# Kernel tuning notes

Measured on AMD Instinct MI355X. Metric: run time of the kernel, lower is better.

Reference implementation:

```python
import jax, jax.numpy as jnp
import numpy as np

N = 32768
E = 524288
B = 128
D = 256


def setup_inputs() -> dict:
    key = jax.random.key(0)
    ks = jax.random.split(key, 8)
    b_z = jax.random.normal(ks[0], (N, D), dtype=jnp.float32)
    src = jax.random.randint(ks[1], (E,), 0, N, dtype=jnp.int32)
    dst = jax.random.randint(ks[2], (E,), 0, N, dtype=jnp.int32)
    b_edge_weight = jax.random.uniform(ks[3], (E,), dtype=jnp.float32)
    # Glorot-ish init for layer weights (256->128->64->1)
    W1 = jax.random.normal(ks[4], (256, 128), dtype=jnp.float32) / np.sqrt(256)
    W2 = jax.random.normal(ks[5], (128, 64), dtype=jnp.float32) / np.sqrt(128)
    W3 = jax.random.normal(ks[6], (64, 1), dtype=jnp.float32) / np.sqrt(64)
    b1 = jnp.zeros((128,), jnp.float32)
    b2 = jnp.zeros((64,), jnp.float32)
    b3 = jnp.zeros((1,), jnp.float32)
    return {"b_z": b_z, "src": src, "dst": dst, "b_edge_weight": b_edge_weight,
            "W1": W1, "b1": b1, "W2": W2, "b2": b2, "W3": W3, "b3": b3,
            "b_size": B}


def _degree_norms(src, dst, n):
    ones = jnp.ones(src.shape[0], jnp.float32)
    out_deg = jax.ops.segment_sum(ones, src, num_segments=n)
    in_deg = jax.ops.segment_sum(ones, dst, num_segments=n)
    # DGL GraphConv norm='both': unweighted degrees, clamped to 1
    return jnp.clip(out_deg, 1.0) ** -0.5, jnp.clip(in_deg, 1.0) ** -0.5


def _gcn_layer(x, src, dst, ew, norm_src, norm_dst, W, b, use_tanh):
    # norm='both': scale source features, transform first (in_feats > out_feats),
    # weighted neighbor sum, then scale by in-degree norm, add bias, activate.
    h = (x * norm_src[:, None]) @ W            # [N, out]
    m = h[src] * ew[:, None]                   # [E, out] gathered messages
    agg = jax.ops.segment_sum(m, dst, num_segments=x.shape[0])  # [N, out]
    out = agg * norm_dst[:, None] + b
    return jnp.tanh(out) if use_tanh else out


def reference(b_z, src, dst, b_edge_weight, W1, b1, W2, b2, W3, b3, b_size):
    norm_src, norm_dst = _degree_norms(src, dst, b_z.shape[0])
    h = _gcn_layer(b_z, src, dst, b_edge_weight, norm_src, norm_dst, W1, b1, True)
    h = _gcn_layer(h, src, dst, b_edge_weight, norm_src, norm_dst, W2, b2, True)
    h = _gcn_layer(h, src, dst, b_edge_weight, norm_src, norm_dst, W3, b3, False)
    return h.reshape(b_size, -1)
```

## Files before the change

kernel.cpp:

```cpp
#include <hip/hip_runtime.h>


#define NB 128
#define NW4 8192

typedef unsigned int uint32;
typedef unsigned short ushort_t;
typedef __attribute__((ext_vector_type(8))) short bf16x8;
typedef __attribute__((ext_vector_type(4))) float f32x4;

__device__ inline ushort_t f2bf(float f) {
  uint32 u = __float_as_uint(f);
  u += 0x7fffu + ((u >> 16) & 1u);
  return (ushort_t)(u >> 16);
}
__device__ inline float bf2f(ushort_t h) { return __uint_as_float(((uint32)h) << 16); }


__global__ __launch_bounds__(1024) void lds_hist_kernel(const int* __restrict__ src,
                                                        const int* __restrict__ dst,
                                                        uint32* __restrict__ part_src,
                                                        uint32* __restrict__ part_dst,
                                                        int e, int epb) {
  __shared__ uint32 hs[NW4];
  __shared__ uint32 hd[NW4];
  const int t = threadIdx.x;
  for (int w = t; w < NW4; w += 1024) {
    hs[w] = 0;
    hd[w] = 0;
  }
  __syncthreads();
  const int base = blockIdx.x * epb;
  for (int k = t; k < epb; k += 1024) {
    int i = base + k;
    if (i < e) {
      int s = src[i], d = dst[i];
      atomicAdd(&hs[s >> 2], 1u << ((s & 3) * 8));
      atomicAdd(&hd[d >> 2], 1u << ((d & 3) * 8));
    }
  }
  __syncthreads();
  uint32* ps = part_src + (size_t)blockIdx.x * NW4;
  uint32* pd = part_dst + (size_t)blockIdx.x * NW4;
  for (int w = t; w < NW4; w += 1024) {
    ps[w] = hs[w];
    pd[w] = hd[w];
  }
}

__global__ void reduce_norm_kernel(const uint32* __restrict__ part_src,
                                   const uint32* __restrict__ part_dst,
                                   float* __restrict__ norm_src, float* __restrict__ norm_dst,
                                   int* __restrict__ in_deg, int n4) {
  int w = blockIdx.x * blockDim.x + threadIdx.x;
  if (w >= n4) return;
  uint32 ss = 0, sd = 0;
  for (int r = 0; r < NB; ++r) {
    ss += part_src[(size_t)r * n4 + w];
    sd += part_dst[(size_t)r * n4 + w];
  }
#pragma unroll
  for (int j = 0; j < 4; ++j) {
    int v = w * 4 + j;
    int od = (ss >> (j * 8)) & 0xff;
    int id = (sd >> (j * 8)) & 0xff;
    norm_src[v] = 1.0f / sqrtf((float)max(od, 1));
    norm_dst[v] = 1.0f / sqrtf((float)max(id, 1));
    in_deg[v] = id;
  }
}

__global__ __launch_bounds__(256) void scan_partials_a(const int* __restrict__ deg,
                                                       int* __restrict__ block_sums, int n) {
  const int t = threadIdx.x;
  const int gid = blockIdx.x * 256 + t;
  int d = (gid < n) ? deg[gid] : 0;
#pragma unroll
  for (int off = 32; off > 0; off >>= 1) d += __shfl_down(d, off, 64);
  __shared__ int wsum[4];
  if ((t & 63) == 0) wsum[t >> 6] = d;
  __syncthreads();
  if (t == 0) block_sums[blockIdx.x] = wsum[0] + wsum[1] + wsum[2] + wsum[3];
}

__global__ __launch_bounds__(256) void scan_partials_b(int* __restrict__ block_sums,
                                                       int* __restrict__ block_offs, int nb) {
  __shared__ int sh[256];
  const int t = threadIdx.x;
  sh[t] = (t < nb) ? block_sums[t] : 0;
  __syncthreads();
  for (int off = 1; off < 256; off <<= 1) {
    int v = sh[t];
    int add = (t >= off) ? sh[t - off] : 0;
    __syncthreads();
    sh[t] = v + add;
    __syncthreads();
  }
  if (t < nb) block_offs[t] = (t > 0) ? sh[t - 1] : 0;
}

__global__ __launch_bounds__(256) void scan_write(const int* __restrict__ deg,
                                                  const int* __restrict__ block_offs,
                                                  int* __restrict__ row_ptr, int n) {
  __shared__ int sh[256];
  const int t = threadIdx.x;
  const int gid = blockIdx.x * 256 + t;
  int d = (gid < n) ? deg[gid] : 0;
  sh[t] = d;
  __syncthreads();
  for (int off = 1; off < 256; off <<= 1) {
    int v = sh[t];
    int add = (t >= off) ? sh[t - off] : 0;
    __syncthreads();
    sh[t] = v + add;
    __syncthreads();
  }
  if (gid < n) {
    int excl = block_offs[blockIdx.x] + sh[t] - d;
    row_ptr[gid] = excl;
    if (gid == n - 1) row_ptr[n] = excl + d;
  }
}

__global__ void group_offs_kernel(const uint32* __restrict__ part_dst,
                                  const int* __restrict__ row_ptr,
                                  int* __restrict__ goff, int n) {
  int v = blockIdx.x * blockDim.x + threadIdx.x;
  if (v >= n) return;
  int base = row_ptr[v];
  const int w = v >> 2;
  const int sh = (v & 3) * 8;
  const int n4 = n >> 2;
  for (int r = 0; r < NB; ++r) {
    goff[(size_t)r * n + v] = base;
    base += (part_dst[(size_t)r * n4 + w] >> sh) & 0xff;
  }
}

__global__ __launch_bounds__(1024) void scatter_kernel(const int* __restrict__ src,
                                                       const int* __restrict__ dst,
                                                       const float* __restrict__ ew,
                                                       const int* __restrict__ goff,
                                                       int2* __restrict__ csr,
                                                       int n, int e, int epb) {
  __shared__ uint32 rk[NW4];
  const int t = threadIdx.x;
  for (int w = t; w < NW4; w += 1024) rk[w] = 0;
  __syncthreads();
  const int base = blockIdx.x * epb;
  const int* gof = goff + (size_t)blockIdx.x * n;
  for (int k = t; k < epb; k += 1024) {
    int i = base + k;
    if (i < e) {
      int d = dst[i];
      uint32 sh = (d & 3) * 8;
      uint32 old = atomicAdd(&rk[d >> 2], 1u << sh);
      int rank = (old >> sh) & 0xff;
      csr[gof[d] + rank] = make_int2(src[i], __float_as_int(ew[i]));
    }
  }
}

__global__ void wsplit_kernel(const float* __restrict__ W, ushort_t* __restrict__ WhT,
                              ushort_t* __restrict__ WlT, int K, int OUT) {
  int i = blockIdx.x * blockDim.x + threadIdx.x;
  if (i >= K * OUT) return;
  int k = i / OUT, c = i % OUT;
  float f = W[i];
  ushort_t h = f2bf(f);
  ushort_t l = f2bf(f - bf2f(h));
  WhT[(size_t)c * K + k] = h;
  WlT[(size_t)c * K + k] = l;
}

template <int K, int OUT>
__global__ __launch_bounds__(256) void gemm_mfma(const float* __restrict__ x,
                                                 const ushort_t* __restrict__ WhT,
                                                 const ushort_t* __restrict__ WlT,
                                                 const float* __restrict__ norm_src,
                                                 ushort_t* __restrict__ ht, int n) {
  constexpr int BK = 64, KP = BK + 8;
  constexpr int NCT = OUT / 32;
  __shared__ ushort_t Xh[64][KP], Xl[64][KP];
  __shared__ ushort_t Wh[OUT][KP], Wl[OUT][KP];

  const int tid = threadIdx.x;
  const int wv = tid >> 6;
  const int lane = tid & 63;
  const int wr = wv >> 1;
  const int wc = wv & 1;
  const int row0 = blockIdx.x * 64;
  const int fr = lane & 15;
  const int fg = lane >> 4;

  f32x4 acc[2][NCT];
#pragma unroll
  for (int i = 0; i < 2; ++i)
#pragma unroll
    for (int j = 0; j < NCT; ++j) acc[i][j] = (f32x4){0.f, 0.f, 0.f, 0.f};

#pragma unroll 1
  for (int k0 = 0; k0 < K; k0 += BK) {
    __syncthreads();
#pragma unroll
    for (int p = 0; p < 4; ++p) {
      int idx = p * 256 + tid;
      int r = idx >> 4, c4 = idx & 15;
      float4 v = *reinterpret_cast<const float4*>(x + (size_t)(row0 + r) * K + k0 + c4 * 4);
      ushort4 h, l;
      h.x = f2bf(v.x); l.x = f2bf(v.x - bf2f(h.x));
      h.y = f2bf(v.y); l.y = f2bf(v.y - bf2f(h.y));
      h.z = f2bf(v.z); l.z = f2bf(v.z - bf2f(h.z));
      h.w = f2bf(v.w); l.w = f2bf(v.w - bf2f(h.w));
      *reinterpret_cast<ushort4*>(&Xh[r][c4 * 4]) = h;
      *reinterpret_cast<ushort4*>(&Xl[r][c4 * 4]) = l;
    }
#pragma unroll
    for (int p = 0; p < OUT * 16 / 256; ++p) {
      int idx = p * 256 + tid;
      int c = idx >> 4, k4 = idx & 15;
      *reinterpret_cast<ushort4*>(&Wh[c][k4 * 4]) =
          *reinterpret_cast<const ushort4*>(WhT + (size_t)c * K + k0 + k4 * 4);
      *reinterpret_cast<ushort4*>(&Wl[c][k4 * 4]) =
          *reinterpret_cast<const ushort4*>(WlT + (size_t)c * K + k0 + k4 * 4);
    }
    __syncthreads();

#pragma unroll
    for (int s = 0; s < 2; ++s) {
      const int kk = s * 32 + fg * 8;
      bf16x8 ah[2], al[2];
#pragma unroll
      for (int i = 0; i < 2; ++i) {
        int r = wr * 32 + i * 16 + fr;
        ah[i] = *reinterpret_cast<const bf16x8*>(&Xh[r][kk]);
        al[i] = *reinterpret_cast<const bf16x8*>(&Xl[r][kk]);
      }
#pragma unroll
      for (int j = 0; j < NCT; ++j) {
        int c = wc * (OUT / 2) + j * 16 + fr;
        bf16x8 bh = *reinterpret_cast<const bf16x8*>(&Wh[c][kk]);
        bf16x8 bl = *reinterpret_cast<const bf16x8*>(&Wl[c][kk]);
#pragma unroll
        for (int i = 0; i < 2; ++i) {
          acc[i][j] = __builtin_amdgcn_mfma_f32_16x16x32_bf16(ah[i], bh, acc[i][j], 0, 0, 0);
          acc[i][j] = __builtin_amdgcn_mfma_f32_16x16x32_bf16(ah[i], bl, acc[i][j], 0, 0, 0);
          acc[i][j] = __builtin_amdgcn_mfma_f32_16x16x32_bf16(al[i], bh, acc[i][j], 0, 0, 0);
        }
      }
    }
  }

#pragma unroll
  for (int i = 0; i < 2; ++i) {
#pragma unroll
    for (int q = 0; q < 4; ++q) {
      int row = row0 + wr * 32 + i * 16 + fg * 4 + q;
      float ns = norm_src[row];
#pragma unroll
      for (int j = 0; j < NCT; ++j) {
        int col = wc * (OUT / 2) + j * 16 + fr;
        ht[(size_t)row * OUT + col] = f2bf(acc[i][j][q] * ns);
      }
    }
  }
}

#define GATHB(e, acc)                                                               \
  {                                                                                 \
    float w_ = __int_as_float(e.y);                                                 \
    ushort4 h_ = *reinterpret_cast<const ushort4*>(ht + (size_t)e.x * OUT + cg * 4);\
    acc.x += w_ * bf2f(h_.x);                                                       \
    acc.y += w_ * bf2f(h_.y);                                                       \
    acc.z += w_ * bf2f(h_.z);                                                       \
    acc.w += w_ * bf2f(h_.w);                                                       \
  }

template <int OUT>
__global__ void aggregate_kernel(const ushort_t* __restrict__ ht, const int* __restrict__ row_ptr,
                                 const int2* __restrict__ csr, const float* __restrict__ norm_dst,
                                 const float* __restrict__ bias, float* __restrict__ out, int n) {
  constexpr int LPN = OUT / 4;
  constexpr int NPB = 256 / LPN;
  const int tid = threadIdx.x;
  const int cg = tid % LPN;
  const int v = blockIdx.x * NPB + tid / LPN;
  if (v >= n) return;

  const int s0 = row_ptr[v];
  const int s1 = row_ptr[v + 1];
  float4 a0 = {0, 0, 0, 0}, a1 = {0, 0, 0, 0}, a2 = {0, 0, 0, 0}, a3 = {0, 0, 0, 0};
  int i = s0;
  for (; i + 4 <= s1; i += 4) {
    int2 e0 = csr[i], e1 = csr[i + 1], e2 = csr[i + 2], e3 = csr[i + 3];
    GATHB(e0, a0);
    GATHB(e1, a1);
    GATHB(e2, a2);
    GATHB(e3, a3);
  }
  for (; i < s1; ++i) {
    int2 e = csr[i];
    GATHB(e, a0);
  }
  float nd = norm_dst[v];
  float4 b4 = *reinterpret_cast<const float4*>(bias + cg * 4);
  float4 r;
  r.x = tanhf((a0.x + a1.x + a2.x + a3.x) * nd + b4.x);
  r.y = tanhf((a0.y + a1.y + a2.y + a3.y) * nd + b4.y);
  r.z = tanhf((a0.z + a1.z + a2.z + a3.z) * nd + b4.z);
  r.w = tanhf((a0.w + a1.w + a2.w + a3.w) * nd + b4.w);
  *reinterpret_cast<float4*>(out + (size_t)v * OUT + cg * 4) = r;
}

__global__ void aggregate2_fuse3(const ushort_t* __restrict__ ht, const int* __restrict__ row_ptr,
                                 const int2* __restrict__ csr, const float* __restrict__ norm_dst,
                                 const float* __restrict__ norm_src, const float* __restrict__ bias,
                                 const float* __restrict__ W3, float* __restrict__ ht3, int n) {
  constexpr int OUT = 64;
  constexpr int LPN = OUT / 4;
  constexpr int NPB = 256 / LPN;
  const int tid = threadIdx.x;
  const int cg = tid % LPN;
  const int v = blockIdx.x * NPB + tid / LPN;
  if (v >= n) return;

  const int s0 = row_ptr[v];
  const int s1 = row_ptr[v + 1];
  float4 a0 = {0, 0, 0, 0}, a1 = {0, 0, 0, 0}, a2 = {0, 0, 0, 0}, a3 = {0, 0, 0, 0};
  int i = s0;
  for (; i + 4 <= s1; i += 4) {
    int2 e0 = csr[i], e1 = csr[i + 1], e2 = csr[i + 2], e3 = csr[i + 3];
    GATHB(e0, a0);
    GATHB(e1, a1);
    GATHB(e2, a2);
    GATHB(e3, a3);
  }
  for (; i < s1; ++i) {
    int2 e = csr[i];
    GATHB(e, a0);
  }
  float nd = norm_dst[v];
  float4 b4 = *reinterpret_cast<const float4*>(bias + cg * 4);
  float ox = tanhf((a0.x + a1.x + a2.x + a3.x) * nd + b4.x);
  float oy = tanhf((a0.y + a1.y + a2.y + a3.y) * nd + b4.y);
  float oz = tanhf((a0.z + a1.z + a2.z + a3.z) * nd + b4.z);
  float ow = tanhf((a0.w + a1.w + a2.w + a3.w) * nd + b4.w);
  float4 w3 = *reinterpret_cast<const float4*>(W3 + cg * 4);
  float p = ox * w3.x + oy * w3.y + oz * w3.z + ow * w3.w;
#pragma unroll
  for (int m = 1; m < 16; m <<= 1) p += __shfl_xor(p, m, 64);
  if (cg == 0) ht3[v] = p * norm_src[v];
}

__global__ void aggregate3_kernel(const float* __restrict__ ht3, const int* __restrict__ row_ptr,
                                  const int2* __restrict__ csr, const float* __restrict__ norm_dst,
                                  const float* __restrict__ b3, float* __restrict__ out, int n) {
  int v = blockIdx.x * blockDim.x + threadIdx.x;
  if (v >= n) return;
  const int s0 = row_ptr[v];
  const int s1 = row_ptr[v + 1];
  float p0 = 0.f, p1 = 0.f, p2 = 0.f, p3 = 0.f;
  int i = s0;
  for (; i + 4 <= s1; i += 4) {
    int2 e0 = csr[i], e1 = csr[i + 1], e2 = csr[i + 2], e3 = csr[i + 3];
    p0 += __int_as_float(e0.y) * ht3[e0.x];
    p1 += __int_as_float(e1.y) * ht3[e1.x];
    p2 += __int_as_float(e2.y) * ht3[e2.x];
    p3 += __int_as_float(e3.y) * ht3[e3.x];
  }
  for (; i < s1; ++i) {
    int2 e = csr[i];
    p0 += __int_as_float(e.y) * ht3[e.x];
  }
  out[v] = (p0 + p1 + p2 + p3) * norm_dst[v] + b3[0];
}

extern "C" void kernel_launch(void* const* d_in, const int* in_sizes, int n_in,
                              void* d_out, int out_size, void* d_ws, size_t ws_size,
                              hipStream_t stream) {
  const float* b_z = (const float*)d_in[0];
  const int* src = (const int*)d_in[1];
  const int* dst = (const int*)d_in[2];
  const float* ew = (const float*)d_in[3];
  const float* W1 = (const float*)d_in[4];
  const float* b1 = (const float*)d_in[5];
  const float* W2 = (const float*)d_in[6];
  const float* b2 = (const float*)d_in[7];
  const float* W3 = (const float*)d_in[8];
  const float* b3 = (const float*)d_in[9];

  const int N = in_sizes[0] / 256;
  const int E = in_sizes[1];
  const int N4 = N / 4;
  const int epb = (E + NB - 1) / NB;

  char* ws = (char*)d_ws;
  size_t off = 0;
  auto alloc = [&](size_t bytes) -> void* {
    void* p = ws + off;
    off += (bytes + 255) & ~(size_t)255;
    return p;
  };

  uint32* part_src = (uint32*)alloc((size_t)NB * N4 * 4);
  uint32* part_dst = (uint32*)alloc((size_t)NB * N4 * 4);
  int* goff = (int*)alloc((size_t)NB * N * 4);
  float* norm_src = (float*)alloc((size_t)N * 4);
  float* norm_dst = (float*)alloc((size_t)N * 4);
  int* in_deg = (int*)alloc((size_t)N * 4);
  int* row_ptr = (int*)alloc((size_t)(N + 1) * 4);
  int* block_sums = (int*)alloc(256 * 4);
  int* block_offs = (int*)alloc(256 * 4);
  int2* csr = (int2*)alloc((size_t)E * 8);
  ushort_t* HT = (ushort_t*)alloc((size_t)N * 128 * 2);
  float* ACT1 = (float*)alloc((size_t)N * 128 * 4);
  float* HT3 = (float*)alloc((size_t)N * 4);
  ushort_t* WhT1 = (ushort_t*)alloc((size_t)256 * 128 * 2);
  ushort_t* WlT1 = (ushort_t*)alloc((size_t)256 * 128 * 2);
  ushort_t* WhT2 = (ushort_t*)alloc((size_t)128 * 64 * 2);
  ushort_t* WlT2 = (ushort_t*)alloc((size_t)128 * 64 * 2);

  const int nBlocks = (N + 255) / 256;

  lds_hist_kernel<<<NB, 1024, 0, stream>>>(src, dst, part_src, part_dst, E, epb);
  reduce_norm_kernel<<<(N4 + 255) / 256, 256, 0, stream>>>(part_src, part_dst, norm_src,
                                                           norm_dst, in_deg, N4);
  scan_partials_a<<<nBlocks, 256, 0, stream>>>(in_deg, block_sums, N);
  scan_partials_b<<<1, 256, 0, stream>>>(block_sums, block_offs, nBlocks);
  scan_write<<<nBlocks, 256, 0, stream>>>(in_deg, block_offs, row_ptr, N);
  group_offs_kernel<<<nBlocks, 256, 0, stream>>>(part_dst, row_ptr, goff, N);
  scatter_kernel<<<NB, 1024, 0, stream>>>(src, dst, ew, goff, csr, N, E, epb);
  wsplit_kernel<<<(256 * 128 + 255) / 256, 256, 0, stream>>>(W1, WhT1, WlT1, 256, 128);
  wsplit_kernel<<<(128 * 64 + 255) / 256, 256, 0, stream>>>(W2, WhT2, WlT2, 128, 64);

  gemm_mfma<256, 128><<<N / 64, 256, 0, stream>>>(b_z, WhT1, WlT1, norm_src, HT, N);
  aggregate_kernel<128><<<(N + 7) / 8, 256, 0, stream>>>(HT, row_ptr, csr, norm_dst, b1, ACT1, N);
  gemm_mfma<128, 64><<<N / 64, 256, 0, stream>>>(ACT1, WhT2, WlT2, norm_src, HT, N);
  aggregate2_fuse3<<<(N + 15) / 16, 256, 0, stream>>>(HT, row_ptr, csr, norm_dst, norm_src, b2,
                                                      W3, HT3, N);
  aggregate3_kernel<<<nBlocks, 256, 0, stream>>>(HT3, row_ptr, csr, norm_dst, b3,
                                                 (float*)d_out, N);
}
```

Before: 124.0 us.

## Restructure CSR build: split degree reduction, fuse scan/group offsets, byte prefixes

The CSR construction pipeline is reworked. The histogram block count doubles to 256, and the partial histograms are reduced in two stages (segmented partial sums, then a final pass) for more parallelism. The block-sum scan step is folded into the norm kernel and the group-offset computation into the scan-write kernel, which drops launches. Per-block offsets are now stored as byte-sized prefixes relative to row_ptr rather than int offsets, cutting memory traffic, and the two weight-split launches merge into one. The risks are more histogram traffic from the larger NB, and uchar prefixes overflow if a node receives 256 or more edges from one block.

After: 111.5 us. 10.1% less time.

```diff
diff --git a/kernel.cpp b/kernel.cpp
--- a/kernel.cpp
+++ b/kernel.cpp
@@ -1,10 +1,12 @@
 #include <hip/hip_runtime.h>
 
 
-#define NB 128
+#define NB 256
 #define NW4 8192
+#define RSEG 8
 
 typedef unsigned int uint32;
+typedef unsigned char uchar_t;
 typedef unsigned short ushort_t;
 typedef __attribute__((ext_vector_type(8))) short bf16x8;
 typedef __attribute__((ext_vector_type(4))) float f32x4;
@@ -16,11 +18,9 @@
 }
 __device__ inline float bf2f(ushort_t h) { return __uint_as_float(((uint32)h) << 16); }
 
-
 __global__ __launch_bounds__(1024) void lds_hist_kernel(const int* __restrict__ src,
                                                         const int* __restrict__ dst,
-                                                        uint32* __restrict__ part_src,
-                                                        uint32* __restrict__ part_dst,
+                                                        uint32* __restrict__ part,
                                                         int e, int epb) {
   __shared__ uint32 hs[NW4];
   __shared__ uint32 hd[NW4];
@@ -40,25 +40,40 @@
     }
   }
   __syncthreads();
-  uint32* ps = part_src + (size_t)blockIdx.x * NW4;
-  uint32* pd = part_dst + (size_t)blockIdx.x * NW4;
+  uint32* ps = part + (size_t)blockIdx.x * NW4;
+  uint32* pd = part + (size_t)(NB + blockIdx.x) * NW4;
   for (int w = t; w < NW4; w += 1024) {
     ps[w] = hs[w];
     pd[w] = hd[w];
   }
 }
 
-__global__ void reduce_norm_kernel(const uint32* __restrict__ part_src,
-                                   const uint32* __restrict__ part_dst,
-                                   float* __restrict__ norm_src, float* __restrict__ norm_dst,
-                                   int* __restrict__ in_deg, int n4) {
-  int w = blockIdx.x * blockDim.x + threadIdx.x;
+__global__ __launch_bounds__(256) void norm_partial(const uint32* __restrict__ part,
+                                                    uint32* __restrict__ psum, int n4) {
+  const int w = blockIdx.x * 256 + threadIdx.x;
+  const int seg = blockIdx.y;
+  const int a = blockIdx.z;
+  const uint32* p = part + (size_t)a * NB * n4 + (size_t)seg * (NB / RSEG) * n4 + w;
+  uint32 s = 0;
+#pragma unroll
+  for (int r = 0; r < NB / RSEG; ++r) s += p[(size_t)r * n4];
+  psum[(size_t)a * RSEG * n4 + (size_t)seg * n4 + w] = s;
+}
+
+__global__ __launch_bounds__(256) void norm_final(const uint32* __restrict__ psum,
+                                                  float* __restrict__ norm_src,
+                                                  float* __restrict__ norm_dst,
+                                                  int* __restrict__ in_deg,
+                                                  int* __restrict__ block_sums, int n4) {
+  const int w = blockIdx.x * 256 + threadIdx.x;
   if (w >= n4) return;
   uint32 ss = 0, sd = 0;
-  for (int r = 0; r < NB; ++r) {
-    ss += part_src[(size_t)r * n4 + w];
-    sd += part_dst[(size_t)r * n4 + w];
-  }
+#pragma unroll
+  for (int seg = 0; seg < RSEG; ++seg) {
+    ss += psum[(size_t)seg * n4 + w];
+    sd += psum[(size_t)(RSEG + seg) * n4 + w];
+  }
+  int idsum = 0;
 #pragma unroll
   for (int j = 0; j < 4; ++j) {
     int v = w * 4 + j;
@@ -67,20 +82,11 @@
     norm_src[v] = 1.0f / sqrtf((float)max(od, 1));
     norm_dst[v] = 1.0f / sqrtf((float)max(id, 1));
     in_deg[v] = id;
-  }
-}
-
-__global__ __launch_bounds__(256) void scan_partials_a(const int* __restrict__ deg,
-                                                       int* __restrict__ block_sums, int n) {
-  const int t = threadIdx.x;
-  const int gid = blockIdx.x * 256 + t;
-  int d = (gid < n) ? deg[gid] : 0;
-#pragma unroll
-  for (int off = 32; off > 0; off >>= 1) d += __shfl_down(d, off, 64);
-  __shared__ int wsum[4];
-  if ((t & 63) == 0) wsum[t >> 6] = d;
-  __syncthreads();
-  if (t == 0) block_sums[blockIdx.x] = wsum[0] + wsum[1] + wsum[2] + wsum[3];
+    idsum += id;
+  }
+#pragma unroll
+  for (int off = 32; off > 0; off >>= 1) idsum += __shfl_down(idsum, off, 64);
+  if ((threadIdx.x & 63) == 0) block_sums[w >> 6] = idsum;
 }
 
 __global__ __launch_bounds__(256) void scan_partials_b(int* __restrict__ block_sums,
@@ -99,13 +105,15 @@
   if (t < nb) block_offs[t] = (t > 0) ? sh[t - 1] : 0;
 }
 
-__global__ __launch_bounds__(256) void scan_write(const int* __restrict__ deg,
-                                                  const int* __restrict__ block_offs,
-                                                  int* __restrict__ row_ptr, int n) {
+__global__ __launch_bounds__(256) void scan_write_goffs(const int* __restrict__ in_deg,
+                                                        const int* __restrict__ block_offs,
+                                                        const uint32* __restrict__ part_dst,
+                                                        int* __restrict__ row_ptr,
+                                                        uchar_t* __restrict__ gpre, int n) {
   __shared__ int sh[256];
   const int t = threadIdx.x;
   const int gid = blockIdx.x * 256 + t;
-  int d = (gid < n) ? deg[gid] : 0;
+  int d = (gid < n) ? in_deg[gid] : 0;
   sh[t] = d;
   __syncthreads();
   for (int off = 1; off < 256; off <<= 1) {
@@ -115,32 +123,26 @@
     sh[t] = v + add;
     __syncthreads();
   }
-  if (gid < n) {
-    int excl = block_offs[blockIdx.x] + sh[t] - d;
-    row_ptr[gid] = excl;
-    if (gid == n - 1) row_ptr[n] = excl + d;
-  }
-}
-
-__global__ void group_offs_kernel(const uint32* __restrict__ part_dst,
-                                  const int* __restrict__ row_ptr,
-                                  int* __restrict__ goff, int n) {
-  int v = blockIdx.x * blockDim.x + threadIdx.x;
-  if (v >= n) return;
-  int base = row_ptr[v];
-  const int w = v >> 2;
-  const int sh = (v & 3) * 8;
+  if (gid >= n) return;
+  int excl = block_offs[blockIdx.x] + sh[t] - d;
+  row_ptr[gid] = excl;
+  if (gid == n - 1) row_ptr[n] = excl + d;
+  const int w = gid >> 2;
+  const int shft = (gid & 3) * 8;
   const int n4 = n >> 2;
+  int cum = 0;
+#pragma unroll 8
   for (int r = 0; r < NB; ++r) {
-    goff[(size_t)r * n + v] = base;
-    base += (part_dst[(size_t)r * n4 + w] >> sh) & 0xff;
+    gpre[(size_t)r * n + gid] = (uchar_t)cum;
+    cum += (part_dst[(size_t)r * n4 + w] >> shft) & 0xff;
   }
 }
 
 __global__ __launch_bounds__(1024) void scatter_kernel(const int* __restrict__ src,
                                                        const int* __restrict__ dst,
                                                        const float* __restrict__ ew,
-                                                       const int* __restrict__ goff,
+                                                       const int* __restrict__ row_ptr,
+                                                       const uchar_t* __restrict__ gpre,
                                                        int2* __restrict__ csr,
                                                        int n, int e, int epb) {
   __shared__ uint32 rk[NW4];
@@ -148,7 +150,7 @@
   for (int w = t; w < NW4; w += 1024) rk[w] = 0;
   __syncthreads();
   const int base = blockIdx.x * epb;
-  const int* gof = goff + (size_t)blockIdx.x * n;
+  const uchar_t* gp = gpre + (size_t)blockIdx.x * n;
   for (int k = t; k < epb; k += 1024) {
     int i = base + k;
     if (i < e) {
@@ -156,21 +158,30 @@
       uint32 sh = (d & 3) * 8;
       uint32 old = atomicAdd(&rk[d >> 2], 1u << sh);
       int rank = (old >> sh) & 0xff;
-      csr[gof[d] + rank] = make_int2(src[i], __float_as_int(ew[i]));
-    }
-  }
-}
-
-__global__ void wsplit_kernel(const float* __restrict__ W, ushort_t* __restrict__ WhT,
-                              ushort_t* __restrict__ WlT, int K, int OUT) {
+      int pos = row_ptr[d] + (int)gp[d] + rank;
+      csr[pos] = make_int2(src[i], __float_as_int(ew[i]));
+    }
+  }
+}
+
+__global__ void wsplit_all(const float* __restrict__ W1, const float* __restrict__ W2,
+                           ushort_t* __restrict__ WhT1, ushort_t* __restrict__ WlT1,
+                           ushort_t* __restrict__ WhT2, ushort_t* __restrict__ WlT2) {
   int i = blockIdx.x * blockDim.x + threadIdx.x;
-  if (i >= K * OUT) return;
-  int k = i / OUT, c = i % OUT;
-  float f = W[i];
-  ushort_t h = f2bf(f);
-  ushort_t l = f2bf(f - bf2f(h));
-  WhT[(size_t)c * K + k] = h;
-  WlT[(size_t)c * K + k] = l;
+  if (i < 256 * 128) {
+    int k = i / 128, c = i % 128;
+    float f = W1[i];
+    ushort_t h = f2bf(f);
+    WhT1[(size_t)c * 256 + k] = h;
+    WlT1[(size_t)c * 256 + k] = f2bf(f - bf2f(h));
+  } else if (i < 256 * 128 + 128 * 64) {
+    int j = i - 256 * 128;
+    int k = j / 64, c = j % 64;
+    float f = W2[j];
+    ushort_t h = f2bf(f);
+    WhT2[(size_t)c * 128 + k] = h;
+    WlT2[(size_t)c * 128 + k] = f2bf(f - bf2f(h));
+  }
 }
 
 template <int K, int OUT>
@@ -402,9 +413,9 @@
     return p;
   };
 
-  uint32* part_src = (uint32*)alloc((size_t)NB * N4 * 4);
-  uint32* part_dst = (uint32*)alloc((size_t)NB * N4 * 4);
-  int* goff = (int*)alloc((size_t)NB * N * 4);
+  uint32* part = (uint32*)alloc((size_t)2 * NB * N4 * 4);
+  uint32* psum = (uint32*)alloc((size_t)2 * RSEG * N4 * 4);
+  uchar_t* gpre = (uchar_t*)alloc((size_t)NB * N);
   float* norm_src = (float*)alloc((size_t)N * 4);
   float* norm_dst = (float*)alloc((size_t)N * 4);
   int* in_deg = (int*)alloc((size_t)N * 4);
@@ -420,18 +431,17 @@
   ushort_t* WhT2 = (ushort_t*)alloc((size_t)128 * 64 * 2);
   ushort_t* WlT2 = (ushort_t*)alloc((size_t)128 * 64 * 2);
 
+  const uint32* part_dst = part + (size_t)NB * N4;
   const int nBlocks = (N + 255) / 256;
 
-  lds_hist_kernel<<<NB, 1024, 0, stream>>>(src, dst, part_src, part_dst, E, epb);
-  reduce_norm_kernel<<<(N4 + 255) / 256, 256, 0, stream>>>(part_src, part_dst, norm_src,
-                                                           norm_dst, in_deg, N4);
-  scan_partials_a<<<nBlocks, 256, 0, stream>>>(in_deg, block_sums, N);
+  lds_hist_kernel<<<NB, 1024, 0, stream>>>(src, dst, part, E, epb);
+  norm_partial<<<dim3(N4 / 256, RSEG, 2), 256, 0, stream>>>(part, psum, N4);
+  norm_final<<<N4 / 256, 256, 0, stream>>>(psum, norm_src, norm_dst, in_deg, block_sums, N4);
   scan_partials_b<<<1, 256, 0, stream>>>(block_sums, block_offs, nBlocks);
-  scan_write<<<nBlocks, 256, 0, stream>>>(in_deg, block_offs, row_ptr, N);
-  group_offs_kernel<<<nBlocks, 256, 0, stream>>>(part_dst, row_ptr, goff, N);
-  scatter_kernel<<<NB, 1024, 0, stream>>>(src, dst, ew, goff, csr, N, E, epb);
-  wsplit_kernel<<<(256 * 128 + 255) / 256, 256, 0, stream>>>(W1, WhT1, WlT1, 256, 128);
-  wsplit_kernel<<<(128 * 64 + 255) / 256, 256, 0, stream>>>(W2, WhT2, WlT2, 128, 64);
+  scan_write_goffs<<<nBlocks, 256, 0, stream>>>(in_deg, block_offs, part_dst, row_ptr, gpre, N);
+  scatter_kernel<<<NB, 1024, 0, stream>>>(src, dst, ew, row_ptr, gpre, csr, N, E, epb);
+  wsplit_all<<<(256 * 128 + 128 * 64 + 255) / 256, 256, 0, stream>>>(W1, W2, WhT1, WlT1,
+                                                                     WhT2, WlT2);
 
   gemm_mfma<256, 128><<<N / 64, 256, 0, stream>>>(b_z, WhT1, WlT1, norm_src, HT, N);
   aggregate_kernel<128><<<(N + 7) / 8, 256, 0, stream>>>(HT, row_ptr, csr, norm_dst, b1, ACT1, N);
```
